# Kernel tuning notes

Hardware: AMD Instinct MI355X
Metric: run time of the kernel (lower is better)

Reference implementation:

```python
import jax, jax.numpy as jnp
import numpy as np

NEG_SLOPE = 0.2


def gat_layer(x, src, dst, W, a_src, a_dst, b, heads, out_c, concat):
    N = x.shape[0]
    h = (x @ W).reshape(N, heads, out_c)                      # [N,H,C]
    alpha_s = jnp.einsum('nhc,hc->nh', h, a_src)              # [N,H]
    alpha_d = jnp.einsum('nhc,hc->nh', h, a_dst)              # [N,H]
    e = jax.nn.leaky_relu(alpha_s[src] + alpha_d[dst], NEG_SLOPE)  # [E,H]
    # softmax over incoming edges per destination node (segment softmax)
    m = jax.ops.segment_max(e, dst, num_segments=N)
    m = jnp.where(jnp.isfinite(m), m, 0.0)
    ex = jnp.exp(e - m[dst])
    denom = jax.ops.segment_sum(ex, dst, num_segments=N)
    alpha = ex / (denom[dst] + 1e-16)                         # [E,H]
    out = jax.ops.segment_sum(alpha[:, :, None] * h[src], dst, num_segments=N)  # [N,H,C]
    out = out.reshape(N, heads * out_c) if concat else out.mean(axis=1)
    return out + b


def setup_inputs() -> dict:
    key = jax.random.key(0)
    ks = jax.random.split(key, 12)
    N, E, D, H, C, G = 20000, 160000, 256, 4, 128, 64
    x = jax.random.normal(ks[0], (N, D), dtype=jnp.float32)
    edge_index = jax.random.randint(ks[1], (2, E), 0, N)
    batch = jnp.sort(jax.random.randint(ks[2], (N,), 0, G))
    s = 0.05
    params = {
        'W1': jax.random.normal(ks[3], (D, H * C), jnp.float32) * s,
        'a_src1': jax.random.normal(ks[4], (H, C), jnp.float32) * s,
        'a_dst1': jax.random.normal(ks[5], (H, C), jnp.float32) * s,
        'b1': jnp.zeros((H * C,), jnp.float32),
        'W2': jax.random.normal(ks[6], (H * C, C), jnp.float32) * s,
        'a_src2': jax.random.normal(ks[7], (1, C), jnp.float32) * s,
        'a_dst2': jax.random.normal(ks[8], (1, C), jnp.float32) * s,
        'b2': jnp.zeros((C,), jnp.float32),
        'fc1_W': jax.random.normal(ks[9], (C, C // 2), jnp.float32) * s,
        'fc1_b': jnp.zeros((C // 2,), jnp.float32),
        'fc2_W': jax.random.normal(ks[10], (C // 2, 1), jnp.float32) * s,
        'fc2_b': jnp.zeros((1,), jnp.float32),
    }
    return dict(x=x, edge_index=edge_index, batch=batch, **params)


def reference(x, edge_index, batch, W1, a_src1, a_dst1, b1, W2, a_src2, a_dst2, b2,
              fc1_W, fc1_b, fc2_W, fc2_b):
    N = x.shape[0]
    G = 64  # number of graphs
    # add self-loops (PyG GATConv default)
    loop = jnp.arange(N, dtype=edge_index.dtype)
    src = jnp.concatenate([edge_index[0], loop])
    dst = jnp.concatenate([edge_index[1], loop])
    h = jax.nn.relu(gat_layer(x, src, dst, W1, a_src1, a_dst1, b1, 4, 128, True))
    h = gat_layer(h, src, dst, W2, a_src2, a_dst2, b2, 1, 128, False)
    # global mean pool per graph
    sums = jax.ops.segment_sum(h, batch, num_segments=G)
    cnts = jax.ops.segment_sum(jnp.ones((N,), h.dtype), batch, num_segments=G)
    pooled = sums / jnp.maximum(cnts, 1.0)[:, None]          # [G,128]
    out = jax.nn.relu(pooled @ fc1_W + fc1_b)
    return out @ fc2_W + fc2_b                                # [G,1]
```

## Files before the change

kernel.cpp:

```cpp
#include <hip/hip_runtime.h>
#include <hip/hip_bf16.h>
#include <cstdint>
#include <cstddef>

#define NEG_SLOPE 0.2f

typedef __attribute__((ext_vector_type(8))) __bf16 bf16x8;
typedef __attribute__((ext_vector_type(4))) __bf16 bf16x4;
typedef __attribute__((ext_vector_type(4))) float  f32x4;

template<int MF, int NF, bool STORE_BF16>
__global__ __launch_bounds__(256) void gemm_mfma(
    const __bf16* __restrict__ A, const __bf16* __restrict__ Bhi,
    const __bf16* __restrict__ Blo, void* __restrict__ Cout,
    int M, int N, int K)
{
    const int tid  = threadIdx.x;
    const int wave = tid >> 6, lane = tid & 63;
    const int wr = wave >> 1, wc = wave & 1;
    const int rowbase = blockIdx.y * (32 * MF) + wr * (16 * MF);
    const int colbase = blockIdx.x * (32 * NF) + wc * (16 * NF);
    const int l15 = lane & 15, kg = lane >> 4;

    size_t aoff[MF], boff[NF];
    #pragma unroll
    for (int mf = 0; mf < MF; ++mf) {
        int r = rowbase + mf * 16 + l15;
        if (r > M - 1) r = M - 1;
        aoff[mf] = (size_t)r * K + kg * 8;
    }
    #pragma unroll
    for (int nf = 0; nf < NF; ++nf) {
        int c = colbase + nf * 16 + l15;
        boff[nf] = (size_t)c * K + kg * 8;
    }

    f32x4 acc[MF][NF];
    #pragma unroll
    for (int mf = 0; mf < MF; ++mf)
        #pragma unroll
        for (int nf = 0; nf < NF; ++nf)
            acc[mf][nf] = (f32x4){0.f, 0.f, 0.f, 0.f};

    #pragma unroll 2
    for (int k0 = 0; k0 < K; k0 += 32) {
        bf16x8 af[MF], bh[NF], bl[NF];
        #pragma unroll
        for (int mf = 0; mf < MF; ++mf)
            af[mf] = *(const bf16x8*)(A + aoff[mf] + k0);
        #pragma unroll
        for (int nf = 0; nf < NF; ++nf) {
            bh[nf] = *(const bf16x8*)(Bhi + boff[nf] + k0);
            bl[nf] = *(const bf16x8*)(Blo + boff[nf] + k0);
        }
        #pragma unroll
        for (int mf = 0; mf < MF; ++mf)
            #pragma unroll
            for (int nf = 0; nf < NF; ++nf) {
                acc[mf][nf] = __builtin_amdgcn_mfma_f32_16x16x32_bf16(af[mf], bh[nf], acc[mf][nf], 0, 0, 0);
                acc[mf][nf] = __builtin_amdgcn_mfma_f32_16x16x32_bf16(af[mf], bl[nf], acc[mf][nf], 0, 0, 0);
            }
    }

    #pragma unroll
    for (int mf = 0; mf < MF; ++mf)
        #pragma unroll
        for (int j = 0; j < 4; ++j) {
            int r = rowbase + mf * 16 + kg * 4 + j;
            if (r < M) {
                #pragma unroll
                for (int nf = 0; nf < NF; ++nf) {
                    int c = colbase + nf * 16 + l15;
                    if (STORE_BF16)
                        ((__bf16*)Cout)[(size_t)r * N + c] = (__bf16)acc[mf][nf][j];
                    else
                        ((float*)Cout)[(size_t)r * N + c] = acc[mf][nf][j];
                }
            }
        }
}

__global__ void cvtw_kernel(const float* __restrict__ W1, const float* __restrict__ W2,
                            __bf16* __restrict__ w1thi, __bf16* __restrict__ w1tlo,
                            __bf16* __restrict__ w2thi, __bf16* __restrict__ w2tlo)
{
    int i = blockIdx.x * 256 + threadIdx.x;
    if (i < 256 * 512) {
        int k = i >> 9, n = i & 511;
        float w = W1[i];
        __bf16 hi = (__bf16)w;
        __bf16 lo = (__bf16)(w - (float)hi);
        w1thi[n * 256 + k] = hi;
        w1tlo[n * 256 + k] = lo;
    } else {
        int j = i - 256 * 512;
        if (j < 512 * 128) {
            int k = j >> 7, n = j & 127;
            float w = W2[j];
            __bf16 hi = (__bf16)w;
            __bf16 lo = (__bf16)(w - (float)hi);
            w2thi[n * 512 + k] = hi;
            w2tlo[n * 512 + k] = lo;
        }
    }
}

__global__ void attvec_kernel(const float* __restrict__ W1, const float* __restrict__ as1w,
                              const float* __restrict__ ad1w, const float* __restrict__ W2,
                              const float* __restrict__ as2w, const float* __restrict__ ad2w,
                              float* __restrict__ wsd1, float* __restrict__ wsd2)
{
    int t = blockIdx.x * 256 + threadIdx.x;
    if (t < 2048) {
        int k = t >> 3, v = t & 7, h = v >> 1;
        const float* av = (v & 1) ? (ad1w + h * 128) : (as1w + h * 128);
        float s = 0.f;
        for (int c = 0; c < 128; ++c) s += W1[k * 512 + h * 128 + c] * av[c];
        wsd1[v * 256 + k] = s;
    } else if (t < 3072) {
        int t2 = t - 2048;
        int k = t2 >> 1, v = t2 & 1;
        const float* av = v ? ad2w : as2w;
        float s = 0.f;
        for (int c = 0; c < 128; ++c) s += W2[k * 128 + c] * av[c];
        wsd2[v * 512 + k] = s;
    }
}

__global__ __launch_bounds__(256) void cvtx_kernel(
    const float* __restrict__ x, const float* __restrict__ wsd1,
    __bf16* __restrict__ xb, float* __restrict__ as1_, float* __restrict__ ad1_, int N)
{
    int wave = threadIdx.x >> 6, lane = threadIdx.x & 63;
    int n = blockIdx.x * 4 + wave;
    if (n >= N) return;
    float4 xv = *(const float4*)&x[(size_t)n * 256 + lane * 4];
    bf16x4 xo;
    xo[0] = (__bf16)xv.x; xo[1] = (__bf16)xv.y; xo[2] = (__bf16)xv.z; xo[3] = (__bf16)xv.w;
    *(bf16x4*)&xb[(size_t)n * 256 + lane * 4] = xo;
    float p[8];
    #pragma unroll
    for (int v = 0; v < 8; ++v) {
        float4 wv = *(const float4*)&wsd1[v * 256 + lane * 4];
        p[v] = xv.x * wv.x + xv.y * wv.y + xv.z * wv.z + xv.w * wv.w;
    }
    #pragma unroll
    for (int v = 0; v < 8; ++v)
        #pragma unroll
        for (int s = 1; s < 64; s <<= 1) p[v] += __shfl_xor(p[v], s);
    if (lane == 0) {
        #pragma unroll
        for (int h = 0; h < 4; ++h) {
            as1_[n * 4 + h] = p[2 * h];
            ad1_[n * 4 + h] = p[2 * h + 1];
        }
    }
}

__global__ void count_kernel(const int* __restrict__ ei, int* __restrict__ cnt,
                             int ET, int E0)
{
    int e = blockIdx.x * blockDim.x + threadIdx.x;
    if (e >= ET) return;
    int d = (e < E0) ? ei[E0 + e] : (e - E0);
    atomicAdd(&cnt[d], 1);
}

__global__ void scan1(const int* __restrict__ cnt, int* __restrict__ offs,
                      int* __restrict__ bsum, int n)
{
    __shared__ int tmp[256];
    int t = threadIdx.x;
    int i = blockIdx.x * 256 + t;
    int v = (i < n) ? cnt[i] : 0;
    tmp[t] = v;
    __syncthreads();
    for (int s = 1; s < 256; s <<= 1) {
        int a = (t >= s) ? tmp[t - s] : 0;
        __syncthreads();
        tmp[t] += a;
        __syncthreads();
    }
    if (i < n) offs[i] = tmp[t] - v;
    if (t == 255) bsum[blockIdx.x] = tmp[255];
}

__global__ void scan2(const int* __restrict__ bsum, int* __restrict__ bofs,
                      int B, int* __restrict__ total_dst)
{
    __shared__ int tmp[256];
    int t = threadIdx.x;
    int v = (t < B) ? bsum[t] : 0;
    tmp[t] = v;
    __syncthreads();
    for (int s = 1; s < 256; s <<= 1) {
        int a = (t >= s) ? tmp[t - s] : 0;
        __syncthreads();
        tmp[t] += a;
        __syncthreads();
    }
    if (t < B) bofs[t] = tmp[t] - v;
    if (t == 255) *total_dst = tmp[255];
}

__global__ void scan3(int* __restrict__ offs, const int* __restrict__ bofs, int n)
{
    int i = blockIdx.x * 256 + threadIdx.x;
    if (i < n) offs[i] += bofs[blockIdx.x];
}

__global__ void scatter_kernel(const int* __restrict__ ei, const int* __restrict__ offs,
                               int* __restrict__ cur, int* __restrict__ eid,
                               int ET, int E0)
{
    int e = blockIdx.x * blockDim.x + threadIdx.x;
    if (e >= ET) return;
    int d   = (e < E0) ? ei[E0 + e] : (e - E0);
    int pos = atomicAdd(&cur[d], 1);
    eid[offs[d] + pos] = e;
}

__global__ __launch_bounds__(128) void aggregate1_kernel(
    const __bf16* __restrict__ h1b, const int* __restrict__ offs,
    const int* __restrict__ eid, const int* __restrict__ ei,
    const float* __restrict__ as1_, const float* __restrict__ ad1_,
    const float* __restrict__ b1, const float* __restrict__ wsd2,
    __bf16* __restrict__ out1b, float* __restrict__ as2_, float* __restrict__ ad2_,
    int E0)
{
    int n = blockIdx.x;
    int t = threadIdx.x;
    int lane = t & 63, wave = t >> 6;
    int hd = t >> 5;
    int l32 = t & 31;
    int s0 = offs[n], s1 = offs[n + 1];
    float adn = ad1_[n * 4 + hd];
    __shared__ float sm_m[4], sm_inv[4];

    float m = -1e30f;
    for (int j = s0 + l32; j < s1; j += 32) {
        int e = eid[j];
        int s = (e < E0) ? ei[e] : (e - E0);
        float v = as1_[s * 4 + hd] + adn;
        v = (v < 0.f) ? NEG_SLOPE * v : v;
        m = fmaxf(m, v);
    }
    #pragma unroll
    for (int s_ = 1; s_ < 32; s_ <<= 1) m = fmaxf(m, __shfl_xor(m, s_));
    float den = 0.f;
    for (int j = s0 + l32; j < s1; j += 32) {
        int e = eid[j];
        int s = (e < E0) ? ei[e] : (e - E0);
        float v = as1_[s * 4 + hd] + adn;
        v = (v < 0.f) ? NEG_SLOPE * v : v;
        den += __expf(v - m);
    }
    #pragma unroll
    for (int s_ = 1; s_ < 32; s_ <<= 1) den += __shfl_xor(den, s_);
    if (l32 == 0) { sm_m[hd] = m; sm_inv[hd] = 1.f / (den + 1e-16f); }
    __syncthreads();
    m = sm_m[hd];
    float inv = sm_inv[hd];

    float a0 = 0.f, a1 = 0.f, a2 = 0.f, a3 = 0.f;
    for (int j = s0; j < s1; ++j) {
        int e = eid[j];
        int s = (e < E0) ? ei[e] : (e - E0);
        float v = as1_[s * 4 + hd] + adn;
        v = (v < 0.f) ? NEG_SLOPE * v : v;
        float w = __expf(v - m) * inv;
        bf16x4 hv = *(const bf16x4*)&h1b[(size_t)s * 512 + t * 4];
        a0 = fmaf(w, (float)hv[0], a0);
        a1 = fmaf(w, (float)hv[1], a1);
        a2 = fmaf(w, (float)hv[2], a2);
        a3 = fmaf(w, (float)hv[3], a3);
    }
    float o0 = fmaxf(a0 + b1[t * 4 + 0], 0.f);
    float o1 = fmaxf(a1 + b1[t * 4 + 1], 0.f);
    float o2 = fmaxf(a2 + b1[t * 4 + 2], 0.f);
    float o3 = fmaxf(a3 + b1[t * 4 + 3], 0.f);
    bf16x4 ov;
    ov[0] = (__bf16)o0; ov[1] = (__bf16)o1; ov[2] = (__bf16)o2; ov[3] = (__bf16)o3;
    *(bf16x4*)&out1b[(size_t)n * 512 + t * 4] = ov;

    float ps = o0 * wsd2[t * 4 + 0] + o1 * wsd2[t * 4 + 1]
             + o2 * wsd2[t * 4 + 2] + o3 * wsd2[t * 4 + 3];
    float pd = o0 * wsd2[512 + t * 4 + 0] + o1 * wsd2[512 + t * 4 + 1]
             + o2 * wsd2[512 + t * 4 + 2] + o3 * wsd2[512 + t * 4 + 3];
    #pragma unroll
    for (int s_ = 1; s_ < 64; s_ <<= 1) {
        ps += __shfl_xor(ps, s_);
        pd += __shfl_xor(pd, s_);
    }
    __shared__ float red[4];
    if (lane == 0) { red[wave * 2] = ps; red[wave * 2 + 1] = pd; }
    __syncthreads();
    if (t == 0) {
        as2_[n] = red[0] + red[2];
        ad2_[n] = red[1] + red[3];
    }
}

__global__ __launch_bounds__(64) void aggregate2_kernel(
    const float* __restrict__ h2, const int* __restrict__ offs,
    const int* __restrict__ eid, const int* __restrict__ ei,
    const float* __restrict__ as2_, const float* __restrict__ ad2_,
    const float* __restrict__ b2, float* __restrict__ out2, int E0)
{
    int n = blockIdx.x, lane = threadIdx.x;
    int s0 = offs[n], s1 = offs[n + 1];
    float adn = ad2_[n];
    float m = -1e30f;
    for (int j = s0 + lane; j < s1; j += 64) {
        int e = eid[j];
        int s = (e < E0) ? ei[e] : (e - E0);
        float v = as2_[s] + adn;
        v = (v < 0.f) ? NEG_SLOPE * v : v;
        m = fmaxf(m, v);
    }
    #pragma unroll
    for (int s_ = 1; s_ < 64; s_ <<= 1) m = fmaxf(m, __shfl_xor(m, s_));
    float den = 0.f;
    for (int j = s0 + lane; j < s1; j += 64) {
        int e = eid[j];
        int s = (e < E0) ? ei[e] : (e - E0);
        float v = as2_[s] + adn;
        v = (v < 0.f) ? NEG_SLOPE * v : v;
        den += __expf(v - m);
    }
    #pragma unroll
    for (int s_ = 1; s_ < 64; s_ <<= 1) den += __shfl_xor(den, s_);
    float inv = 1.f / (den + 1e-16f);

    float a0 = 0.f, a1 = 0.f;
    for (int j = s0; j < s1; ++j) {
        int e = eid[j];
        int s = (e < E0) ? ei[e] : (e - E0);
        float v = as2_[s] + adn;
        v = (v < 0.f) ? NEG_SLOPE * v : v;
        float w = __expf(v - m) * inv;
        float2 hv = *(const float2*)&h2[(size_t)s * 128 + lane * 2];
        a0 = fmaf(w, hv.x, a0);
        a1 = fmaf(w, hv.y, a1);
    }
    float2 o;
    o.x = a0 + b2[lane * 2 + 0];
    o.y = a1 + b2[lane * 2 + 1];
    *(float2*)&out2[(size_t)n * 128 + lane * 2] = o;
}

__global__ void gstart_kernel(const int* __restrict__ batch, int* __restrict__ gstart,
                              int N, int G)
{
    int n = blockIdx.x * blockDim.x + threadIdx.x;
    if (n >= N) return;
    int b    = batch[n];
    int prev = (n == 0) ? -1 : batch[n - 1];
    for (int g = prev + 1; g <= b; ++g) gstart[g] = n;
    if (n == N - 1) {
        for (int g = b + 1; g <= G; ++g) gstart[g] = N;
    }
}

#define POOL_S 16
__global__ void pool_stage1(const float* __restrict__ out2, const int* __restrict__ gstart,
                            float* __restrict__ partial, int C)
{
    int g = blockIdx.x, slice = blockIdx.y;
    int c = threadIdx.x;
    int s = gstart[g], e = gstart[g + 1];
    int len = e - s;
    int chunk = (len + POOL_S - 1) / POOL_S;
    int n0 = s + slice * chunk;
    int n1 = min(n0 + chunk, e);
    float acc = 0.f;
    for (int n = n0; n < n1; ++n) acc += out2[(size_t)n * C + c];
    partial[((size_t)g * POOL_S + slice) * C + c] = acc;
}

__global__ void pool_stage2(const float* __restrict__ partial, const int* __restrict__ gstart,
                            float* __restrict__ pooled, int C)
{
    int g = blockIdx.x;
    int c = threadIdx.x;
    float acc = 0.f;
    #pragma unroll
    for (int s = 0; s < POOL_S; ++s)
        acc += partial[((size_t)g * POOL_S + s) * C + c];
    float cntf = (float)(gstart[g + 1] - gstart[g]);
    pooled[(size_t)g * C + c] = acc / fmaxf(cntf, 1.0f);
}

__global__ void head_kernel(const float* __restrict__ pooled, const float* __restrict__ fc1W,
                            const float* __restrict__ fc1b, const float* __restrict__ fc2W,
                            const float* __restrict__ fc2b, float* __restrict__ out)
{
    int g = blockIdx.x;
    int j = threadIdx.x;
    float t = 0.f;
    for (int c = 0; c < 128; ++c)
        t += pooled[(size_t)g * 128 + c] * fc1W[c * 64 + j];
    t = fmaxf(t + fc1b[j], 0.f);
    float v = t * fc2W[j];
    #pragma unroll
    for (int s = 32; s > 0; s >>= 1) v += __shfl_down(v, s);
    if (j == 0) out[g] = v + fc2b[0];
}

extern "C" void kernel_launch(void* const* d_in, const int* in_sizes, int n_in,
                              void* d_out, int out_size, void* d_ws, size_t ws_size,
                              hipStream_t stream)
{
    const float* x    = (const float*)d_in[0];
    const int*   ei   = (const int*)d_in[1];
    const int*   batch= (const int*)d_in[2];
    const float* W1   = (const float*)d_in[3];
    const float* as1w = (const float*)d_in[4];
    const float* ad1w = (const float*)d_in[5];
    const float* b1   = (const float*)d_in[6];
    const float* W2   = (const float*)d_in[7];
    const float* as2w = (const float*)d_in[8];
    const float* ad2w = (const float*)d_in[9];
    const float* b2   = (const float*)d_in[10];
    const float* fc1W = (const float*)d_in[11];
    const float* fc1b = (const float*)d_in[12];
    const float* fc2W = (const float*)d_in[13];
    const float* fc2b = (const float*)d_in[14];
    float* out = (float*)d_out;

    const int D = 256, H1 = 4, C = 128, HC = 512, G = 64;
    const int N  = in_sizes[0] / D;
    const int E0 = in_sizes[1] / 2;
    const int ET = E0 + N;
    const int NB = (N + 255) / 256;

    char* p = (char*)d_ws;
    auto alloc = [&](size_t bytes) -> char* {
        char* r = p;
        p += (bytes + 255) & ~(size_t)255;
        return r;
    };
    __bf16* xb    = (__bf16*)alloc((size_t)N * D * 2);
    float*  h2    = (float*)xb;
    __bf16* h1b   = (__bf16*)alloc((size_t)N * HC * 2);
    float*  out2  = (float*)h1b;
    __bf16* out1b = (__bf16*)alloc((size_t)N * HC * 2);
    __bf16* w1thi = (__bf16*)alloc((size_t)256 * 512 * 2);
    __bf16* w1tlo = (__bf16*)alloc((size_t)256 * 512 * 2);
    __bf16* w2thi = (__bf16*)alloc((size_t)512 * 128 * 2);
    __bf16* w2tlo = (__bf16*)alloc((size_t)512 * 128 * 2);
    float* wsd1 = (float*)alloc(8 * 256 * 4);
    float* wsd2 = (float*)alloc(2 * 512 * 4);
    float* as1_ = (float*)alloc((size_t)N * 4 * 4);
    float* ad1_ = (float*)alloc((size_t)N * 4 * 4);
    float* as2_ = (float*)alloc((size_t)N * 4);
    float* ad2_ = (float*)alloc((size_t)N * 4);
    int*   cnt    = (int*)alloc((size_t)N * 4);
    int*   cur    = (int*)alloc((size_t)N * 4);
    int*   offs   = (int*)alloc((size_t)(N + 1) * 4);
    int*   eid    = (int*)alloc((size_t)ET * 4);
    int*   bsum   = (int*)alloc(256 * 4);
    int*   bofs   = (int*)alloc(256 * 4);
    int*   gstart = (int*)alloc((size_t)(G + 1) * 4);
    float* partial= (float*)alloc((size_t)G * POOL_S * C * 4);
    float* pooled = (float*)alloc((size_t)G * C * 4);

    hipMemsetAsync(cnt, 0, (size_t)N * 4, stream);
    hipMemsetAsync(cur, 0, (size_t)N * 4, stream);
    count_kernel<<<(ET + 255) / 256, 256, 0, stream>>>(ei, cnt, ET, E0);
    scan1<<<NB, 256, 0, stream>>>(cnt, offs, bsum, N);
    scan2<<<1, 256, 0, stream>>>(bsum, bofs, NB, offs + N);
    scan3<<<NB, 256, 0, stream>>>(offs, bofs, N);
    scatter_kernel<<<(ET + 255) / 256, 256, 0, stream>>>(ei, offs, cur, eid, ET, E0);

    cvtw_kernel<<<(256 * 512 + 512 * 128 + 255) / 256, 256, 0, stream>>>(
        W1, W2, w1thi, w1tlo, w2thi, w2tlo);
    attvec_kernel<<<12, 256, 0, stream>>>(W1, as1w, ad1w, W2, as2w, ad2w, wsd1, wsd2);
    cvtx_kernel<<<N / 4, 256, 0, stream>>>(x, wsd1, xb, as1_, ad1_, N);

    gemm_mfma<4, 4, true><<<dim3(HC / 128, (N + 127) / 128), 256, 0, stream>>>(
        xb, w1thi, w1tlo, h1b, N, HC, D);
    aggregate1_kernel<<<N, 128, 0, stream>>>(
        h1b, offs, eid, ei, as1_, ad1_, b1, wsd2, out1b, as2_, ad2_, E0);

    gemm_mfma<2, 2, false><<<dim3(C / 64, (N + 63) / 64), 256, 0, stream>>>(
        out1b, w2thi, w2tlo, h2, N, C, HC);
    aggregate2_kernel<<<N, 64, 0, stream>>>(
        h2, offs, eid, ei, as2_, ad2_, b2, out2, E0);

    gstart_kernel<<<(N + 255) / 256, 256, 0, stream>>>(batch, gstart, N, G);
    pool_stage1<<<dim3(G, POOL_S), C, 0, stream>>>(out2, gstart, partial, C);
    pool_stage2<<<G, C, 0, stream>>>(partial, gstart, pooled, C);
    head_kernel<<<G, 64, 0, stream>>>(pooled, fc1W, fc1b, fc2W, fc2b, out);
}
```

Before: 229.0 us.

## Map one wavefront per node in GAT aggregation, unroll edges, store h2 as bf16

Both aggregation kernels now process one destination node per 64-lane wavefront with four nodes per 256-thread block. This removes the shared-memory softmax broadcast and the block barriers. Layer-1 lanes each handle 8 channels with 16-byte bf16 loads, and both gather loops are unrolled by four edges so more independent loads are in flight. The second GEMM now writes h2 in bf16, halving gather traffic at some precision cost, and h2/out2 get their own buffers instead of aliasing earlier ones.

```diff
diff --git a/kernel.cpp b/kernel.cpp
--- a/kernel.cpp
+++ b/kernel.cpp
@@ -7,6 +7,7 @@
 
 typedef __attribute__((ext_vector_type(8))) __bf16 bf16x8;
 typedef __attribute__((ext_vector_type(4))) __bf16 bf16x4;
+typedef __attribute__((ext_vector_type(2))) __bf16 bf16x2;
 typedef __attribute__((ext_vector_type(4))) float  f32x4;
 
 template<int MF, int NF, bool STORE_BF16>
@@ -220,25 +221,24 @@
     eid[offs[d] + pos] = e;
 }
 
-__global__ __launch_bounds__(128) void aggregate1_kernel(
+__global__ __launch_bounds__(256) void aggregate1_kernel(
     const __bf16* __restrict__ h1b, const int* __restrict__ offs,
     const int* __restrict__ eid, const int* __restrict__ ei,
     const float* __restrict__ as1_, const float* __restrict__ ad1_,
     const float* __restrict__ b1, const float* __restrict__ wsd2,
     __bf16* __restrict__ out1b, float* __restrict__ as2_, float* __restrict__ ad2_,
-    int E0)
-{
-    int n = blockIdx.x;
-    int t = threadIdx.x;
-    int lane = t & 63, wave = t >> 6;
-    int hd = t >> 5;
-    int l32 = t & 31;
+    int E0, int N)
+{
+    int wave = threadIdx.x >> 6, lane = threadIdx.x & 63;
+    int n = blockIdx.x * 4 + wave;
+    if (n >= N) return;
+    int hd  = lane >> 4;
+    int l16 = lane & 15;
     int s0 = offs[n], s1 = offs[n + 1];
     float adn = ad1_[n * 4 + hd];
-    __shared__ float sm_m[4], sm_inv[4];
 
     float m = -1e30f;
-    for (int j = s0 + l32; j < s1; j += 32) {
+    for (int j = s0 + l16; j < s1; j += 16) {
         int e = eid[j];
         int s = (e < E0) ? ei[e] : (e - E0);
         float v = as1_[s * 4 + hd] + adn;
@@ -246,9 +246,9 @@
         m = fmaxf(m, v);
     }
     #pragma unroll
-    for (int s_ = 1; s_ < 32; s_ <<= 1) m = fmaxf(m, __shfl_xor(m, s_));
+    for (int t = 1; t < 16; t <<= 1) m = fmaxf(m, __shfl_xor(m, t));
     float den = 0.f;
-    for (int j = s0 + l32; j < s1; j += 32) {
+    for (int j = s0 + l16; j < s1; j += 16) {
         int e = eid[j];
         int s = (e < E0) ? ei[e] : (e - E0);
         float v = as1_[s * 4 + hd] + adn;
@@ -256,60 +256,86 @@
         den += __expf(v - m);
     }
     #pragma unroll
-    for (int s_ = 1; s_ < 32; s_ <<= 1) den += __shfl_xor(den, s_);
-    if (l32 == 0) { sm_m[hd] = m; sm_inv[hd] = 1.f / (den + 1e-16f); }
-    __syncthreads();
-    m = sm_m[hd];
-    float inv = sm_inv[hd];
-
-    float a0 = 0.f, a1 = 0.f, a2 = 0.f, a3 = 0.f;
-    for (int j = s0; j < s1; ++j) {
+    for (int t = 1; t < 16; t <<= 1) den += __shfl_xor(den, t);
+    float inv = 1.f / (den + 1e-16f);
+
+    float a[8] = {0.f, 0.f, 0.f, 0.f, 0.f, 0.f, 0.f, 0.f};
+    const __bf16* hbase = h1b + lane * 8;
+    int j = s0;
+    for (; j + 3 < s1; j += 4) {
+        int e0 = eid[j], e1 = eid[j + 1], e2 = eid[j + 2], e3 = eid[j + 3];
+        int sA = (e0 < E0) ? ei[e0] : (e0 - E0);
+        int sB = (e1 < E0) ? ei[e1] : (e1 - E0);
+        int sC = (e2 < E0) ? ei[e2] : (e2 - E0);
+        int sD = (e3 < E0) ? ei[e3] : (e3 - E0);
+        float vA = as1_[sA * 4 + hd] + adn;
+        float vB = as1_[sB * 4 + hd] + adn;
+        float vC = as1_[sC * 4 + hd] + adn;
+        float vD = as1_[sD * 4 + hd] + adn;
+        bf16x8 hA = *(const bf16x8*)(hbase + (size_t)sA * 512);
+        bf16x8 hB = *(const bf16x8*)(hbase + (size_t)sB * 512);
+        bf16x8 hC = *(const bf16x8*)(hbase + (size_t)sC * 512);
+        bf16x8 hD = *(const bf16x8*)(hbase + (size_t)sD * 512);
+        vA = (vA < 0.f) ? NEG_SLOPE * vA : vA;
+        vB = (vB < 0.f) ? NEG_SLOPE * vB : vB;
+        vC = (vC < 0.f) ? NEG_SLOPE * vC : vC;
+        vD = (vD < 0.f) ? NEG_SLOPE * vD : vD;
+        float wA = __expf(vA - m) * inv;
+        float wB = __expf(vB - m) * inv;
+        float wC = __expf(vC - m) * inv;
+        float wD = __expf(vD - m) * inv;
+        #pragma unroll
+        for (int i = 0; i < 8; ++i) {
+            a[i] = fmaf(wA, (float)hA[i], a[i]);
+            a[i] = fmaf(wB, (float)hB[i], a[i]);
+            a[i] = fmaf(wC, (float)hC[i], a[i]);
+            a[i] = fmaf(wD, (float)hD[i], a[i]);
+        }
+    }
+    for (; j < s1; ++j) {
         int e = eid[j];
         int s = (e < E0) ? ei[e] : (e - E0);
         float v = as1_[s * 4 + hd] + adn;
         v = (v < 0.f) ? NEG_SLOPE * v : v;
         float w = __expf(v - m) * inv;
-        bf16x4 hv = *(const bf16x4*)&h1b[(size_t)s * 512 + t * 4];
-        a0 = fmaf(w, (float)hv[0], a0);
-        a1 = fmaf(w, (float)hv[1], a1);
-        a2 = fmaf(w, (float)hv[2], a2);
-        a3 = fmaf(w, (float)hv[3], a3);
-    }
-    float o0 = fmaxf(a0 + b1[t * 4 + 0], 0.f);
-    float o1 = fmaxf(a1 + b1[t * 4 + 1], 0.f);
-    float o2 = fmaxf(a2 + b1[t * 4 + 2], 0.f);
-    float o3 = fmaxf(a3 + b1[t * 4 + 3], 0.f);
-    bf16x4 ov;
-    ov[0] = (__bf16)o0; ov[1] = (__bf16)o1; ov[2] = (__bf16)o2; ov[3] = (__bf16)o3;
-    *(bf16x4*)&out1b[(size_t)n * 512 + t * 4] = ov;
-
-    float ps = o0 * wsd2[t * 4 + 0] + o1 * wsd2[t * 4 + 1]
-             + o2 * wsd2[t * 4 + 2] + o3 * wsd2[t * 4 + 3];
-    float pd = o0 * wsd2[512 + t * 4 + 0] + o1 * wsd2[512 + t * 4 + 1]
-             + o2 * wsd2[512 + t * 4 + 2] + o3 * wsd2[512 + t * 4 + 3];
-    #pragma unroll
-    for (int s_ = 1; s_ < 64; s_ <<= 1) {
-        ps += __shfl_xor(ps, s_);
-        pd += __shfl_xor(pd, s_);
-    }
-    __shared__ float red[4];
-    if (lane == 0) { red[wave * 2] = ps; red[wave * 2 + 1] = pd; }
-    __syncthreads();
-    if (t == 0) {
-        as2_[n] = red[0] + red[2];
-        ad2_[n] = red[1] + red[3];
-    }
-}
-
-__global__ __launch_bounds__(64) void aggregate2_kernel(
-    const float* __restrict__ h2, const int* __restrict__ offs,
+        bf16x8 hv = *(const bf16x8*)(hbase + (size_t)s * 512);
+        #pragma unroll
+        for (int i = 0; i < 8; ++i) a[i] = fmaf(w, (float)hv[i], a[i]);
+    }
+
+    bf16x8 ov;
+    float ps = 0.f, pd = 0.f;
+    #pragma unroll
+    for (int i = 0; i < 8; ++i) {
+        float o = fmaxf(a[i] + b1[lane * 8 + i], 0.f);
+        ov[i] = (__bf16)o;
+        ps = fmaf(o, wsd2[lane * 8 + i], ps);
+        pd = fmaf(o, wsd2[512 + lane * 8 + i], pd);
+    }
+    *(bf16x8*)&out1b[(size_t)n * 512 + lane * 8] = ov;
+    #pragma unroll
+    for (int t = 1; t < 64; t <<= 1) {
+        ps += __shfl_xor(ps, t);
+        pd += __shfl_xor(pd, t);
+    }
+    if (lane == 0) {
+        as2_[n] = ps;
+        ad2_[n] = pd;
+    }
+}
+
+__global__ __launch_bounds__(256) void aggregate2_kernel(
+    const __bf16* __restrict__ h2b, const int* __restrict__ offs,
     const int* __restrict__ eid, const int* __restrict__ ei,
     const float* __restrict__ as2_, const float* __restrict__ ad2_,
-    const float* __restrict__ b2, float* __restrict__ out2, int E0)
-{
-    int n = blockIdx.x, lane = threadIdx.x;
+    const float* __restrict__ b2, float* __restrict__ out2, int E0, int N)
+{
+    int wave = threadIdx.x >> 6, lane = threadIdx.x & 63;
+    int n = blockIdx.x * 4 + wave;
+    if (n >= N) return;
     int s0 = offs[n], s1 = offs[n + 1];
     float adn = ad2_[n];
+
     float m = -1e30f;
     for (int j = s0 + lane; j < s1; j += 64) {
         int e = eid[j];
@@ -319,7 +345,7 @@
         m = fmaxf(m, v);
     }
     #pragma unroll
-    for (int s_ = 1; s_ < 64; s_ <<= 1) m = fmaxf(m, __shfl_xor(m, s_));
+    for (int t = 1; t < 64; t <<= 1) m = fmaxf(m, __shfl_xor(m, t));
     float den = 0.f;
     for (int j = s0 + lane; j < s1; j += 64) {
         int e = eid[j];
@@ -329,19 +355,48 @@
         den += __expf(v - m);
     }
     #pragma unroll
-    for (int s_ = 1; s_ < 64; s_ <<= 1) den += __shfl_xor(den, s_);
+    for (int t = 1; t < 64; t <<= 1) den += __shfl_xor(den, t);
     float inv = 1.f / (den + 1e-16f);
 
     float a0 = 0.f, a1 = 0.f;
-    for (int j = s0; j < s1; ++j) {
+    const __bf16* hbase = h2b + lane * 2;
+    int j = s0;
+    for (; j + 3 < s1; j += 4) {
+        int e0 = eid[j], e1 = eid[j + 1], e2 = eid[j + 2], e3 = eid[j + 3];
+        int sA = (e0 < E0) ? ei[e0] : (e0 - E0);
+        int sB = (e1 < E0) ? ei[e1] : (e1 - E0);
+        int sC = (e2 < E0) ? ei[e2] : (e2 - E0);
+        int sD = (e3 < E0) ? ei[e3] : (e3 - E0);
+        float vA = as2_[sA] + adn;
+        float vB = as2_[sB] + adn;
+        float vC = as2_[sC] + adn;
+        float vD = as2_[sD] + adn;
+        bf16x2 hA = *(const bf16x2*)(hbase + (size_t)sA * 128);
+        bf16x2 hB = *(const bf16x2*)(hbase + (size_t)sB * 128);
+        bf16x2 hC = *(const bf16x2*)(hbase + (size_t)sC * 128);
+        bf16x2 hD = *(const bf16x2*)(hbase + (size_t)sD * 128);
+        vA = (vA < 0.f) ? NEG_SLOPE * vA : vA;
+        vB = (vB < 0.f) ? NEG_SLOPE * vB : vB;
+        vC = (vC < 0.f) ? NEG_SLOPE * vC : vC;
+        vD = (vD < 0.f) ? NEG_SLOPE * vD : vD;
+        float wA = __expf(vA - m) * inv;
+        float wB = __expf(vB - m) * inv;
+        float wC = __expf(vC - m) * inv;
+        float wD = __expf(vD - m) * inv;
+        a0 = fmaf(wA, (float)hA[0], a0); a1 = fmaf(wA, (float)hA[1], a1);
+        a0 = fmaf(wB, (float)hB[0], a0); a1 = fmaf(wB, (float)hB[1], a1);
+        a0 = fmaf(wC, (float)hC[0], a0); a1 = fmaf(wC, (float)hC[1], a1);
+        a0 = fmaf(wD, (float)hD[0], a0); a1 = fmaf(wD, (float)hD[1], a1);
+    }
+    for (; j < s1; ++j) {
         int e = eid[j];
         int s = (e < E0) ? ei[e] : (e - E0);
         float v = as2_[s] + adn;
         v = (v < 0.f) ? NEG_SLOPE * v : v;
         float w = __expf(v - m) * inv;
-        float2 hv = *(const float2*)&h2[(size_t)s * 128 + lane * 2];
-        a0 = fmaf(w, hv.x, a0);
-        a1 = fmaf(w, hv.y, a1);
+        bf16x2 hv = *(const bf16x2*)(hbase + (size_t)s * 128);
+        a0 = fmaf(w, (float)hv[0], a0);
+        a1 = fmaf(w, (float)hv[1], a1);
     }
     float2 o;
     o.x = a0 + b2[lane * 2 + 0];
@@ -428,7 +483,7 @@
     const float* fc2b = (const float*)d_in[14];
     float* out = (float*)d_out;
 
-    const int D = 256, H1 = 4, C = 128, HC = 512, G = 64;
+    const int D = 256, C = 128, HC = 512, G = 64;
     const int N  = in_sizes[0] / D;
     const int E0 = in_sizes[1] / 2;
     const int ET = E0 + N;
@@ -441,10 +496,10 @@
         return r;
     };
     __bf16* xb    = (__bf16*)alloc((size_t)N * D * 2);
-    float*  h2    = (float*)xb;
     __bf16* h1b   = (__bf16*)alloc((size_t)N * HC * 2);
-    float*  out2  = (float*)h1b;
     __bf16* out1b = (__bf16*)alloc((size_t)N * HC * 2);
+    __bf16* h2b   = (__bf16*)alloc((size_t)N * C * 2);
+    float*  out2  = (float*)alloc((size_t)N * C * 4);
     __bf16* w1thi = (__bf16*)alloc((size_t)256 * 512 * 2);
     __bf16* w1tlo = (__bf16*)alloc((size_t)256 * 512 * 2);
     __bf16* w2thi = (__bf16*)alloc((size_t)512 * 128 * 2);
@@ -480,13 +535,13 @@
 
     gemm_mfma<4, 4, true><<<dim3(HC / 128, (N + 127) / 128), 256, 0, stream>>>(
         xb, w1thi, w1tlo, h1b, N, HC, D);
-    aggregate1_kernel<<<N, 128, 0, stream>>>(
-        h1b, offs, eid, ei, as1_, ad1_, b1, wsd2, out1b, as2_, ad2_, E0);
-
-    gemm_mfma<2, 2, false><<<dim3(C / 64, (N + 63) / 64), 256, 0, stream>>>(
-        out1b, w2thi, w2tlo, h2, N, C, HC);
-    aggregate2_kernel<<<N, 64, 0, stream>>>(
-        h2, offs, eid, ei, as2_, ad2_, b2, out2, E0);
+    aggregate1_kernel<<<(N + 3) / 4, 256, 0, stream>>>(
+        h1b, offs, eid, ei, as1_, ad1_, b1, wsd2, out1b, as2_, ad2_, E0, N);
+
+    gemm_mfma<2, 2, true><<<dim3(C / 64, (N + 63) / 64), 256, 0, stream>>>(
+        out1b, w2thi, w2tlo, h2b, N, C, HC);
+    aggregate2_kernel<<<(N + 3) / 4, 256, 0, stream>>>(
+        h2b, offs, eid, ei, as2_, ad2_, b2, out2, E0, N);
 
     gstart_kernel<<<(N + 255) / 256, 256, 0, stream>>>(batch, gstart, N, G);
     pool_stage1<<<dim3(G, POOL_S), C, 0, stream>>>(out2, gstart, partial, C);
```

Result: faster. 212.7 us (-7.1%).
